# Performance work log

Hardware: AMD Instinct MI355X
Metric: run time of the kernel (lower is better)

## Reference

```python
import jax, jax.numpy as jnp
import numpy as np

C0, C1, C2 = 2000, 10000, 50000  # class cutoffs
D = 1024                          # input_size (hidden dim)
OUT_HEAD = C0 + 2                 # head output: shortlist + 2 cluster logits


def setup_inputs() -> dict:
    key = jax.random.key(0)
    ks = jax.random.split(key, 7)
    s = lambda fan_in: 1.0 / np.sqrt(fan_in)
    x = jax.random.normal(ks[0], (4096, D), dtype=jnp.float32)
    Wh = jax.random.normal(ks[1], (OUT_HEAD, D), dtype=jnp.float32) * s(D)
    bh = jnp.zeros((OUT_HEAD,), dtype=jnp.float32)
    # tail 0: D -> D//4**0 -> (C1-C0)
    W0a = jax.random.normal(ks[2], (D, D), dtype=jnp.float32) * s(D)
    W0b = jax.random.normal(ks[3], (C1 - C0, D), dtype=jnp.float32) * s(D)
    # tail 1: D -> D//4**1 -> (C2-C1)
    W1a = jax.random.normal(ks[4], (D // 4, D), dtype=jnp.float32) * s(D)
    W1b = jax.random.normal(ks[5], (C2 - C1, D // 4), dtype=jnp.float32) * s(D // 4)
    return {"x": x, "Wh": Wh, "bh": bh, "W0a": W0a, "W0b": W0b, "W1a": W1a, "W1b": W1b}


def reference(x, Wh, bh, W0a, W0b, W1a, W1b):
    # head: [B, OUT_HEAD]; log-softmax over shortlist + cluster logits
    lsm_head = jax.nn.log_softmax(x @ Wh.T + bh, axis=-1)
    # tail clusters: capacity-reduction linear, projection, log-softmax within cluster
    lsm_t0 = jax.nn.log_softmax((x @ W0a.T) @ W0b.T, axis=-1)  # [B, C1-C0]
    lsm_t1 = jax.nn.log_softmax((x @ W1a.T) @ W1b.T, axis=-1)  # [B, C2-C1]
    # flat log-probs: cluster log-prob broadcast-added to within-cluster log-probs
    prob = jnp.concatenate([
        lsm_head[:, :C0],
        lsm_head[:, C0:C0 + 1] + lsm_t0,
        lsm_head[:, C0 + 1:C0 + 2] + lsm_t1,
    ], axis=1)  # [B, C2]
    return prob
```

## Files before the change

### kernel.cpp

```cpp
#include <hip/hip_runtime.h>
#include <hip/hip_bf16.h>
#include <math.h>

#define CC0 2000
#define CC1 10000
#define CC2 50000
#define DH  1024
#define BATCH 4096
#define OUT_HEAD (CC0 + 2)

#define N0_P 8192
#define N1_P 40192
#define NH_P 2048

typedef __attribute__((ext_vector_type(4))) float  f32x4;
typedef __attribute__((ext_vector_type(8))) __bf16 bf16x8;
typedef __attribute__((ext_vector_type(8))) short  s16x8;

__device__ __forceinline__ void gload_lds16(const void* g, void* l) {
    __builtin_amdgcn_global_load_lds(
        (const __attribute__((address_space(1))) void*)g,
        (__attribute__((address_space(3))) void*)l, 16, 0, 0);
}

__global__ __launch_bounds__(256) void convert_all_kernel(
    const float4* __restrict__ s0, ushort4* __restrict__ d0, int n0s, int n0d,
    const float4* __restrict__ s1, ushort4* __restrict__ d1, int n1s, int n1d,
    const float4* __restrict__ s2, ushort4* __restrict__ d2, int n2s, int n2d,
    const float4* __restrict__ s3, ushort4* __restrict__ d3, int n3s, int n3d,
    const float4* __restrict__ s4, ushort4* __restrict__ d4, int n4s, int n4d,
    const float4* __restrict__ s5, ushort4* __restrict__ d5, int n5s, int n5d,
    float* __restrict__ rs0, float* __restrict__ rs1)
{
    if (blockIdx.y == 6) {
        int i = blockIdx.x * blockDim.x + threadIdx.x;
        if (i < BATCH) { rs0[i] = 0.f; rs1[i] = 0.f; }
        return;
    }
    const float4* src; ushort4* dst; int ns, nd;
    switch (blockIdx.y) {
        case 0: src = s0; dst = d0; ns = n0s; nd = n0d; break;
        case 1: src = s1; dst = d1; ns = n1s; nd = n1d; break;
        case 2: src = s2; dst = d2; ns = n2s; nd = n2d; break;
        case 3: src = s3; dst = d3; ns = n3s; nd = n3d; break;
        case 4: src = s4; dst = d4; ns = n4s; nd = n4d; break;
        default: src = s5; dst = d5; ns = n5s; nd = n5d; break;
    }
    int i = blockIdx.x * blockDim.x + threadIdx.x;
    const int stride = gridDim.x * blockDim.x;
    for (; i < nd; i += stride) {
        ushort4 o = {0, 0, 0, 0};
        if (i < ns) {
            float4 v = src[i];
            o.x = __builtin_bit_cast(unsigned short, (__bf16)v.x);
            o.y = __builtin_bit_cast(unsigned short, (__bf16)v.y);
            o.z = __builtin_bit_cast(unsigned short, (__bf16)v.z);
            o.w = __builtin_bit_cast(unsigned short, (__bf16)v.w);
        }
        dst[i] = o;
    }
}

__global__ __launch_bounds__(256) void gemm128x3_kernel(
    const ushort* __restrict__ x_bf,
    const ushort* __restrict__ W0a_bf, ushort* __restrict__ h0,
    const ushort* __restrict__ W1a_bf, ushort* __restrict__ h1,
    const ushort* __restrict__ Wh_bf,  float*  __restrict__ headL)
{
    __shared__ ushort As[128 * 64];
    __shared__ ushort Bs[128 * 64];

    const int gb = blockIdx.x;
    const ushort* B; void* C;
    int N, ldC, wmode, nbx, lin;
    const int K = DH;
    if (gb < 256)      { B = W0a_bf; C = h0;    N = DH;       ldC = DH;       wmode = 1; nbx = 8;  lin = gb; }
    else if (gb < 320) { B = W1a_bf; C = h1;    N = 256;      ldC = 256;      wmode = 1; nbx = 2;  lin = gb - 256; }
    else               { B = Wh_bf;  C = headL; N = OUT_HEAD; ldC = OUT_HEAD; wmode = 2; nbx = 16; lin = gb - 320; }

    const int nwg = nbx * 32;
    const int q = nwg >> 3;
    int bid = (lin & 7) * q + (lin >> 3);
    const int bx = bid % nbx;
    const int by = bid / nbx;

    const int t = threadIdx.x;
    const int lane = t & 63;
    const int w = t >> 6;
    const int wr = w >> 1, wc = w & 1;
    const int lr = lane & 15;
    const int lg = lane >> 4;
    const int bm = by * 128;
    const int bn = bx * 128;
    const int lrow = lane >> 3;
    const int lcol = (lane & 7) * 8;

    f32x4 acc[4][4] = {};

    for (int k0 = 0; k0 < K; k0 += 64) {
        #pragma unroll
        for (int i = 0; i < 4; ++i) {
            const int seg = w * 4 + i;
            const int row = seg * 8 + lrow;
            gload_lds16(x_bf + (size_t)(bm + row) * K + k0 + lcol, &As[seg * 512]);
            gload_lds16(B + (size_t)(bn + row) * K + k0 + lcol, &Bs[seg * 512]);
        }
        __syncthreads();
        #pragma unroll
        for (int ks = 0; ks < 2; ++ks) {
            s16x8 af[4], bfr[4];
            #pragma unroll
            for (int m = 0; m < 4; ++m)
                af[m] = *(const s16x8*)&As[(wr * 64 + m * 16 + lr) * 64 + ks * 32 + lg * 8];
            #pragma unroll
            for (int n = 0; n < 4; ++n)
                bfr[n] = *(const s16x8*)&Bs[(wc * 64 + n * 16 + lr) * 64 + ks * 32 + lg * 8];
            #pragma unroll
            for (int m = 0; m < 4; ++m)
                #pragma unroll
                for (int n = 0; n < 4; ++n)
                    acc[m][n] = __builtin_amdgcn_mfma_f32_16x16x32_bf16(
                        __builtin_bit_cast(bf16x8, af[m]),
                        __builtin_bit_cast(bf16x8, bfr[n]), acc[m][n], 0, 0, 0);
        }
        __syncthreads();
    }

    #pragma unroll
    for (int m = 0; m < 4; ++m)
        #pragma unroll
        for (int r = 0; r < 4; ++r) {
            const int row = bm + wr * 64 + m * 16 + lg * 4 + r;
            #pragma unroll
            for (int n = 0; n < 4; ++n) {
                const int col = bn + wc * 64 + n * 16 + lr;
                float v = acc[m][n][r];
                if (col < N) {
                    if (wmode == 1)
                        ((ushort*)C)[(size_t)row * ldC + col] =
                            __builtin_bit_cast(unsigned short, (__bf16)v);
                    else
                        ((float*)C)[(size_t)row * ldC + col] = v;
                }
            }
        }
}

__global__ __launch_bounds__(512, 1) void tails256_kernel(
    const ushort* __restrict__ h0, const ushort* __restrict__ W0b,
    ushort* __restrict__ L0, float* __restrict__ rs0,
    const ushort* __restrict__ h1, const ushort* __restrict__ W1b,
    ushort* __restrict__ L1, float* __restrict__ rs1)
{
    __shared__ ushort lds[2][2][256 * 64];

    const int gb = blockIdx.x;
    const ushort *A, *B; ushort* C; float* rsum;
    int K, N, nbx, ldC, lin;
    if (gb < 512) { A = h0; B = W0b; C = L0; rsum = rs0; K = DH;  N = CC1 - CC0; nbx = N0_P / 256; ldC = N0_P; lin = gb; }
    else          { A = h1; B = W1b; C = L1; rsum = rs1; K = 256; N = CC2 - CC1; nbx = N1_P / 256; ldC = N1_P; lin = gb - 512; }

    const int nwg = nbx * 16;
    const int q8 = nwg >> 3;
    int bid = (lin & 7) * q8 + (lin >> 3);
    const int by = bid % 16;
    const int bx = bid / 16;
    const int bm = by * 256, bn = bx * 256;

    const int t = threadIdx.x;
    const int lane = t & 63;
    const int w = t >> 6;
    const int wr = w >> 2;
    const int wc = w & 3;
    const int lr = lane & 15;
    const int lg = lane >> 4;
    const int xr = (lr & 7) << 4;
    const int c0 = w * 64 + lane;

    f32x4 acc[8][4] = {};
    const int nkt = K / 64;

    auto stage_chunk = [&](int ktile, int buf, int p) {
        const int k0 = ktile * 64;
        const int mat = (p == 1 || p == 2) ? 1 : 0;
        const int j = p >> 1;
        const ushort* gbase = mat ? B : A;
        const int brow = mat ? bn : bm;
        #pragma unroll
        for (int i = 0; i < 2; ++i) {
            const int v = i * 512 + c0;
            const int vrow = v >> 3;
            int ar;
            if (mat == 0) ar = ((vrow >> 6) << 7) + (j << 6) + (vrow & 63);
            else          ar = ((vrow >> 5) << 6) + (j << 5) + (vrow & 31);
            const int cc = (v & 7) ^ (ar & 7);
            const int v0 = (i * 512 + w * 64) >> 3;
            int ar0;
            if (mat == 0) ar0 = ((v0 >> 6) << 7) + (j << 6) + (v0 & 63);
            else          ar0 = ((v0 >> 5) << 6) + (j << 5) + (v0 & 31);
            gload_lds16(gbase + (size_t)(brow + ar) * K + k0 + cc * 8,
                        (char*)&lds[buf][mat][0] + ar0 * 128);
        }
    };

    #pragma unroll
    for (int p = 0; p < 4; ++p) stage_chunk(0, 0, p);
    asm volatile("s_waitcnt vmcnt(0)" ::: "memory");
    __builtin_amdgcn_s_barrier();
    asm volatile("" ::: "memory");

    for (int tk = 0; tk < nkt; ++tk) {
        const int cur = tk & 1;
        const char* baseA = (const char*)&lds[cur][0][0];
        const char* baseB = (const char*)&lds[cur][1][0];
        const bool more = (tk + 1 < nkt);
        #pragma unroll
        for (int p = 0; p < 4; ++p) {
            const int mh = p >> 1, nh = p & 1;
            if (more) {
                stage_chunk(tk + 1, cur ^ 1, p);
                asm volatile("s_waitcnt vmcnt(6)" ::: "memory");
            } else {
                if (p == 0)      asm volatile("s_waitcnt vmcnt(4)" ::: "memory");
                else if (p == 1) asm volatile("s_waitcnt vmcnt(2)" ::: "memory");
                else if (p == 2) asm volatile("s_waitcnt vmcnt(0)" ::: "memory");
            }
            __builtin_amdgcn_s_barrier();
            asm volatile("" ::: "memory");

            s16x8 af[4][2], bq[2][2];
            #pragma unroll
            for (int m_ = 0; m_ < 4; ++m_) {
                const int row = wr * 128 + (mh * 4 + m_) * 16 + lr;
                #pragma unroll
                for (int ks = 0; ks < 2; ++ks)
                    af[m_][ks] = *(const s16x8*)(baseA + (row * 128 + ((ks * 64 + lg * 16) ^ xr)));
            }
            #pragma unroll
            for (int n_ = 0; n_ < 2; ++n_) {
                const int row = wc * 64 + (nh * 2 + n_) * 16 + lr;
                #pragma unroll
                for (int ks = 0; ks < 2; ++ks)
                    bq[n_][ks] = *(const s16x8*)(baseB + (row * 128 + ((ks * 64 + lg * 16) ^ xr)));
            }
            __builtin_amdgcn_s_setprio(1);
            #pragma unroll
            for (int m_ = 0; m_ < 4; ++m_)
                #pragma unroll
                for (int n_ = 0; n_ < 2; ++n_)
                    #pragma unroll
                    for (int ks = 0; ks < 2; ++ks)
                        acc[mh * 4 + m_][nh * 2 + n_] = __builtin_amdgcn_mfma_f32_16x16x32_bf16(
                            __builtin_bit_cast(bf16x8, af[m_][ks]),
                            __builtin_bit_cast(bf16x8, bq[n_][ks]),
                            acc[mh * 4 + m_][nh * 2 + n_], 0, 0, 0);
            __builtin_amdgcn_s_setprio(0);
        }
    }

    #pragma unroll
    for (int m = 0; m < 8; ++m) {
        #pragma unroll
        for (int r = 0; r < 4; ++r) {
            const int row = bm + wr * 128 + m * 16 + lg * 4 + r;
            float psum = 0.f;
            #pragma unroll
            for (int n = 0; n < 4; ++n) {
                const int col = bn + wc * 64 + n * 16 + lr;
                float v = acc[m][n][r];
                if (col < N) {
                    C[(size_t)row * ldC + col] =
                        __builtin_bit_cast(unsigned short, (__bf16)v);
                    psum += __expf(v);
                }
            }
            #pragma unroll
            for (int mm = 1; mm < 16; mm <<= 1) psum += __shfl_xor(psum, mm, 64);
            if (lr == 0) atomicAdd(&rsum[row], psum);
        }
    }
}

__global__ __launch_bounds__(256) void head_lsm_kernel(
    const float* __restrict__ HL, const float* __restrict__ bh,
    float* __restrict__ out, float* __restrict__ s01)
{
    const int row = blockIdx.x;
    const float* L = HL + (size_t)row * OUT_HEAD;
    const int t = threadIdx.x;
    __shared__ float red[4];

    float m = -1e30f;
    for (int i = t; i < OUT_HEAD; i += 256) m = fmaxf(m, L[i] + bh[i]);
    #pragma unroll
    for (int s = 1; s < 64; s <<= 1) m = fmaxf(m, __shfl_xor(m, s, 64));
    if ((t & 63) == 0) red[t >> 6] = m;
    __syncthreads();
    m = fmaxf(fmaxf(red[0], red[1]), fmaxf(red[2], red[3]));

    float sum = 0.f;
    for (int i = t; i < OUT_HEAD; i += 256) sum += __expf(L[i] + bh[i] - m);
    #pragma unroll
    for (int s = 1; s < 64; s <<= 1) sum += __shfl_xor(sum, s, 64);
    __syncthreads();
    if ((t & 63) == 0) red[t >> 6] = sum;
    __syncthreads();
    const float lse = m + logf(red[0] + red[1] + red[2] + red[3]);

    float* orow = out + (size_t)row * CC2;
    for (int i = t; i < CC0; i += 256) orow[i] = L[i] + bh[i] - lse;
    if (t == 0) {
        s01[2 * row + 0] = L[CC0 + 0] + bh[CC0 + 0] - lse;
        s01[2 * row + 1] = L[CC0 + 1] + bh[CC0 + 1] - lse;
    }
}

__global__ __launch_bounds__(256) void prep_add_kernel(
    const float* __restrict__ s01, const float* __restrict__ rs0,
    const float* __restrict__ rs1, float* __restrict__ add0,
    float* __restrict__ add1, int n)
{
    int i = blockIdx.x * blockDim.x + threadIdx.x;
    if (i < n) {
        add0[i] = s01[2 * i + 0] - logf(rs0[i]);
        add1[i] = s01[2 * i + 1] - logf(rs1[i]);
    }
}

__global__ __launch_bounds__(256) void finalize_all_kernel(
    const ushort* __restrict__ L0, const ushort* __restrict__ L1,
    const float* __restrict__ add0, const float* __restrict__ add1,
    float* __restrict__ out)
{
    const int row = blockIdx.y;
    const int c = blockIdx.x * blockDim.x + threadIdx.x;
    const ushort* src; float* dst; float add;
    if (c < 1000) {
        src = L0 + (size_t)row * N0_P + c * 8;
        dst = out + (size_t)row * CC2 + CC0 + c * 8;
        add = add0[row];
    } else if (c < 6000) {
        const int c1 = c - 1000;
        src = L1 + (size_t)row * N1_P + c1 * 8;
        dst = out + (size_t)row * CC2 + CC1 + c1 * 8;
        add = add1[row];
    } else return;
    s16x8 v = *(const s16x8*)src;
    float4 o0, o1;
    o0.x = __builtin_bit_cast(float, (unsigned)(unsigned short)v[0] << 16) + add;
    o0.y = __builtin_bit_cast(float, (unsigned)(unsigned short)v[1] << 16) + add;
    o0.z = __builtin_bit_cast(float, (unsigned)(unsigned short)v[2] << 16) + add;
    o0.w = __builtin_bit_cast(float, (unsigned)(unsigned short)v[3] << 16) + add;
    o1.x = __builtin_bit_cast(float, (unsigned)(unsigned short)v[4] << 16) + add;
    o1.y = __builtin_bit_cast(float, (unsigned)(unsigned short)v[5] << 16) + add;
    o1.z = __builtin_bit_cast(float, (unsigned)(unsigned short)v[6] << 16) + add;
    o1.w = __builtin_bit_cast(float, (unsigned)(unsigned short)v[7] << 16) + add;
    *(float4*)dst = o0;
    *(float4*)(dst + 4) = o1;
}

extern "C" void kernel_launch(void* const* d_in, const int* in_sizes, int n_in,
                              void* d_out, int out_size, void* d_ws, size_t ws_size,
                              hipStream_t stream) {
    const float* x   = (const float*)d_in[0];
    const float* Wh  = (const float*)d_in[1];
    const float* bh  = (const float*)d_in[2];
    const float* W0a = (const float*)d_in[3];
    const float* W0b = (const float*)d_in[4];
    const float* W1a = (const float*)d_in[5];
    const float* W1b = (const float*)d_in[6];
    float* out = (float*)d_out;
    char*  ws  = (char*)d_ws;

    size_t off = 0;
    auto alloc = [&](size_t bytes) { size_t o = off; off += (bytes + 255) & ~(size_t)255; return o; };
    ushort* x_bf   = (ushort*)(ws + alloc((size_t)BATCH * DH * 2));
    ushort* Wh_bf  = (ushort*)(ws + alloc((size_t)NH_P * DH * 2));
    ushort* W0a_bf = (ushort*)(ws + alloc((size_t)DH * DH * 2));
    ushort* W0b_bf = (ushort*)(ws + alloc((size_t)N0_P * DH * 2));
    ushort* W1a_bf = (ushort*)(ws + alloc((size_t)256 * DH * 2));
    ushort* W1b_bf = (ushort*)(ws + alloc((size_t)N1_P * 256 * 2));
    ushort* h0_bf  = (ushort*)(ws + alloc((size_t)BATCH * DH * 2));
    ushort* h1_bf  = (ushort*)(ws + alloc((size_t)BATCH * 256 * 2));
    float*  headL  = (float*)(ws + alloc((size_t)BATCH * OUT_HEAD * 4));
    float*  s01    = (float*)(ws + alloc((size_t)BATCH * 2 * 4));
    float*  rs0    = (float*)(ws + alloc((size_t)BATCH * 4));
    float*  rs1    = (float*)(ws + alloc((size_t)BATCH * 4));
    float*  add0   = (float*)(ws + alloc((size_t)BATCH * 4));
    float*  add1   = (float*)(ws + alloc((size_t)BATCH * 4));
    ushort* L0     = (ushort*)(ws + alloc((size_t)BATCH * N0_P * 2));
    ushort* L1     = (ushort*)(ws + alloc((size_t)BATCH * N1_P * 2));

    convert_all_kernel<<<dim3(1280, 7), 256, 0, stream>>>(
        (const float4*)x,   (ushort4*)x_bf,   BATCH * DH / 4,        BATCH * DH / 4,
        (const float4*)Wh,  (ushort4*)Wh_bf,  OUT_HEAD * DH / 4,     NH_P * DH / 4,
        (const float4*)W0a, (ushort4*)W0a_bf, DH * DH / 4,           DH * DH / 4,
        (const float4*)W0b, (ushort4*)W0b_bf, (CC1 - CC0) * DH / 4,  N0_P * DH / 4,
        (const float4*)W1a, (ushort4*)W1a_bf, 256 * DH / 4,          256 * DH / 4,
        (const float4*)W1b, (ushort4*)W1b_bf, (CC2 - CC1) * 256 / 4, N1_P * 256 / 4,
        rs0, rs1);

    gemm128x3_kernel<<<832, 256, 0, stream>>>(
        x_bf, W0a_bf, h0_bf, W1a_bf, h1_bf, Wh_bf, headL);

    head_lsm_kernel<<<BATCH, 256, 0, stream>>>(headL, bh, out, s01);

    tails256_kernel<<<512 + (N1_P / 256) * 16, 512, 0, stream>>>(
        h0_bf, W0b_bf, L0, rs0, h1_bf, W1b_bf, L1, rs1);

    prep_add_kernel<<<(BATCH + 255) / 256, 256, 0, stream>>>(s01, rs0, rs1, add0, add1, BATCH);

    finalize_all_kernel<<<dim3(24, BATCH), 256, 0, stream>>>(L0, L1, add0, add1, out);
}
```

Before: 606.1 us.

## Move tail exp-sum out of GEMM epilogue into a per-row finalize kernel

The tail GEMM no longer computes exp and atomically accumulates row sums in its epilogue. A new per-row finalize kernel reads the bf16 logits, reduces the exp-sum, computes the log-normaliser and writes the output, replacing the prep_add and finalize kernels and the zero-init blocks. The GEMM inner loop also keeps B fragments across the four sub-steps, so A and B are not re-read from LDS. This removes atomics and epilogue transcendental work, but each row's logits are now read twice in the finalize pass and sums are taken over bf16-rounded values.

Result: no change. 600.4 us (-0.9%).

```diff
diff --git a/kernel.cpp b/kernel.cpp
--- a/kernel.cpp
+++ b/kernel.cpp
@@ -29,14 +29,8 @@
     const float4* __restrict__ s2, ushort4* __restrict__ d2, int n2s, int n2d,
     const float4* __restrict__ s3, ushort4* __restrict__ d3, int n3s, int n3d,
     const float4* __restrict__ s4, ushort4* __restrict__ d4, int n4s, int n4d,
-    const float4* __restrict__ s5, ushort4* __restrict__ d5, int n5s, int n5d,
-    float* __restrict__ rs0, float* __restrict__ rs1)
+    const float4* __restrict__ s5, ushort4* __restrict__ d5, int n5s, int n5d)
 {
-    if (blockIdx.y == 6) {
-        int i = blockIdx.x * blockDim.x + threadIdx.x;
-        if (i < BATCH) { rs0[i] = 0.f; rs1[i] = 0.f; }
-        return;
-    }
     const float4* src; ushort4* dst; int ns, nd;
     switch (blockIdx.y) {
         case 0: src = s0; dst = d0; ns = n0s; nd = n0d; break;
@@ -148,17 +142,17 @@
 
 __global__ __launch_bounds__(512, 1) void tails256_kernel(
     const ushort* __restrict__ h0, const ushort* __restrict__ W0b,
-    ushort* __restrict__ L0, float* __restrict__ rs0,
+    ushort* __restrict__ L0,
     const ushort* __restrict__ h1, const ushort* __restrict__ W1b,
-    ushort* __restrict__ L1, float* __restrict__ rs1)
+    ushort* __restrict__ L1)
 {
     __shared__ ushort lds[2][2][256 * 64];
 
     const int gb = blockIdx.x;
-    const ushort *A, *B; ushort* C; float* rsum;
+    const ushort *A, *B; ushort* C;
     int K, N, nbx, ldC, lin;
-    if (gb < 512) { A = h0; B = W0b; C = L0; rsum = rs0; K = DH;  N = CC1 - CC0; nbx = N0_P / 256; ldC = N0_P; lin = gb; }
-    else          { A = h1; B = W1b; C = L1; rsum = rs1; K = 256; N = CC2 - CC1; nbx = N1_P / 256; ldC = N1_P; lin = gb - 512; }
+    if (gb < 512) { A = h0; B = W0b; C = L0; K = DH;  N = CC1 - CC0; nbx = N0_P / 256; ldC = N0_P; lin = gb; }
+    else          { A = h1; B = W1b; C = L1; K = 256; N = CC2 - CC1; nbx = N1_P / 256; ldC = N1_P; lin = gb - 512; }
 
     const int nwg = nbx * 16;
     const int q8 = nwg >> 3;
@@ -183,7 +177,7 @@
     auto stage_chunk = [&](int ktile, int buf, int p) {
         const int k0 = ktile * 64;
         const int mat = (p == 1 || p == 2) ? 1 : 0;
-        const int j = p >> 1;
+        const int j = (p == 3) ? 1 : (p == 2 ? 1 : 0);
         const ushort* gbase = mat ? B : A;
         const int brow = mat ? bn : bm;
         #pragma unroll
@@ -214,6 +208,10 @@
         const char* baseA = (const char*)&lds[cur][0][0];
         const char* baseB = (const char*)&lds[cur][1][0];
         const bool more = (tk + 1 < nkt);
+
+        s16x8 bq[4][2];
+        s16x8 af[4][2];
+
         #pragma unroll
         for (int p = 0; p < 4; ++p) {
             const int mh = p >> 1, nh = p & 1;
@@ -228,20 +226,23 @@
             __builtin_amdgcn_s_barrier();
             asm volatile("" ::: "memory");
 
-            s16x8 af[4][2], bq[2][2];
-            #pragma unroll
-            for (int m_ = 0; m_ < 4; ++m_) {
-                const int row = wr * 128 + (mh * 4 + m_) * 16 + lr;
+            if (p == 0 || p == 2) {
                 #pragma unroll
-                for (int ks = 0; ks < 2; ++ks)
-                    af[m_][ks] = *(const s16x8*)(baseA + (row * 128 + ((ks * 64 + lg * 16) ^ xr)));
+                for (int m_ = 0; m_ < 4; ++m_) {
+                    const int row = wr * 128 + (mh * 4 + m_) * 16 + lr;
+                    #pragma unroll
+                    for (int ks = 0; ks < 2; ++ks)
+                        af[m_][ks] = *(const s16x8*)(baseA + (row * 128 + ((ks * 64 + lg * 16) ^ xr)));
+                }
             }
-            #pragma unroll
-            for (int n_ = 0; n_ < 2; ++n_) {
-                const int row = wc * 64 + (nh * 2 + n_) * 16 + lr;
+            if (p == 0 || p == 1) {
                 #pragma unroll
-                for (int ks = 0; ks < 2; ++ks)
-                    bq[n_][ks] = *(const s16x8*)(baseB + (row * 128 + ((ks * 64 + lg * 16) ^ xr)));
+                for (int n_ = 0; n_ < 2; ++n_) {
+                    const int row = wc * 64 + (p * 2 + n_) * 16 + lr;
+                    #pragma unroll
+                    for (int ks = 0; ks < 2; ++ks)
+                        bq[p * 2 + n_][ks] = *(const s16x8*)(baseB + (row * 128 + ((ks * 64 + lg * 16) ^ xr)));
+                }
             }
             __builtin_amdgcn_s_setprio(1);
             #pragma unroll
@@ -252,7 +253,7 @@
                     for (int ks = 0; ks < 2; ++ks)
                         acc[mh * 4 + m_][nh * 2 + n_] = __builtin_amdgcn_mfma_f32_16x16x32_bf16(
                             __builtin_bit_cast(bf16x8, af[m_][ks]),
-                            __builtin_bit_cast(bf16x8, bq[n_][ks]),
+                            __builtin_bit_cast(bf16x8, bq[nh * 2 + n_][ks]),
                             acc[mh * 4 + m_][nh * 2 + n_], 0, 0, 0);
             __builtin_amdgcn_s_setprio(0);
         }
@@ -263,20 +264,13 @@
         #pragma unroll
         for (int r = 0; r < 4; ++r) {
             const int row = bm + wr * 128 + m * 16 + lg * 4 + r;
-            float psum = 0.f;
             #pragma unroll
             for (int n = 0; n < 4; ++n) {
                 const int col = bn + wc * 64 + n * 16 + lr;
-                float v = acc[m][n][r];
-                if (col < N) {
+                if (col < N)
                     C[(size_t)row * ldC + col] =
-                        __builtin_bit_cast(unsigned short, (__bf16)v);
-                    psum += __expf(v);
-                }
+                        __builtin_bit_cast(unsigned short, (__bf16)acc[m][n][r]);
             }
-            #pragma unroll
-            for (int mm = 1; mm < 16; mm <<= 1) psum += __shfl_xor(psum, mm, 64);
-            if (lr == 0) atomicAdd(&rsum[row], psum);
         }
     }
 }
@@ -315,48 +309,65 @@
     }
 }
 
-__global__ __launch_bounds__(256) void prep_add_kernel(
-    const float* __restrict__ s01, const float* __restrict__ rs0,
-    const float* __restrict__ rs1, float* __restrict__ add0,
-    float* __restrict__ add1, int n)
+__global__ __launch_bounds__(512) void finalize_rows_kernel(
+    const ushort* __restrict__ L0, const ushort* __restrict__ L1,
+    const float* __restrict__ s01, float* __restrict__ out)
 {
-    int i = blockIdx.x * blockDim.x + threadIdx.x;
-    if (i < n) {
-        add0[i] = s01[2 * i + 0] - logf(rs0[i]);
-        add1[i] = s01[2 * i + 1] - logf(rs1[i]);
-    }
-}
-
-__global__ __launch_bounds__(256) void finalize_all_kernel(
-    const ushort* __restrict__ L0, const ushort* __restrict__ L1,
-    const float* __restrict__ add0, const float* __restrict__ add1,
-    float* __restrict__ out)
-{
-    const int row = blockIdx.y;
-    const int c = blockIdx.x * blockDim.x + threadIdx.x;
-    const ushort* src; float* dst; float add;
-    if (c < 1000) {
-        src = L0 + (size_t)row * N0_P + c * 8;
-        dst = out + (size_t)row * CC2 + CC0 + c * 8;
-        add = add0[row];
-    } else if (c < 6000) {
-        const int c1 = c - 1000;
-        src = L1 + (size_t)row * N1_P + c1 * 8;
-        dst = out + (size_t)row * CC2 + CC1 + c1 * 8;
-        add = add1[row];
-    } else return;
-    s16x8 v = *(const s16x8*)src;
-    float4 o0, o1;
-    o0.x = __builtin_bit_cast(float, (unsigned)(unsigned short)v[0] << 16) + add;
-    o0.y = __builtin_bit_cast(float, (unsigned)(unsigned short)v[1] << 16) + add;
-    o0.z = __builtin_bit_cast(float, (unsigned)(unsigned short)v[2] << 16) + add;
-    o0.w = __builtin_bit_cast(float, (unsigned)(unsigned short)v[3] << 16) + add;
-    o1.x = __builtin_bit_cast(float, (unsigned)(unsigned short)v[4] << 16) + add;
-    o1.y = __builtin_bit_cast(float, (unsigned)(unsigned short)v[5] << 16) + add;
-    o1.z = __builtin_bit_cast(float, (unsigned)(unsigned short)v[6] << 16) + add;
-    o1.w = __builtin_bit_cast(float, (unsigned)(unsigned short)v[7] << 16) + add;
-    *(float4*)dst = o0;
-    *(float4*)(dst + 4) = o1;
+    const int row = blockIdx.x;
+    const int t = threadIdx.x;
+    const ushort* r0 = L0 + (size_t)row * N0_P;
+    const ushort* r1 = L1 + (size_t)row * N1_P;
+
+    float p0 = 0.f, p1 = 0.f;
+    for (int c = t; c < 1000; c += 512) {
+        s16x8 v = *(const s16x8*)(r0 + c * 8);
+        #pragma unroll
+        for (int j = 0; j < 8; ++j)
+            p0 += __expf(__builtin_bit_cast(float, (unsigned)(unsigned short)v[j] << 16));
+    }
+    for (int c = t; c < 5000; c += 512) {
+        s16x8 v = *(const s16x8*)(r1 + c * 8);
+        #pragma unroll
+        for (int j = 0; j < 8; ++j)
+            p1 += __expf(__builtin_bit_cast(float, (unsigned)(unsigned short)v[j] << 16));
+    }
+    #pragma unroll
+    for (int s = 1; s < 64; s <<= 1) {
+        p0 += __shfl_xor(p0, s, 64);
+        p1 += __shfl_xor(p1, s, 64);
+    }
+    __shared__ float red0[8], red1[8], bc[2];
+    if ((t & 63) == 0) { red0[t >> 6] = p0; red1[t >> 6] = p1; }
+    __syncthreads();
+    if (t == 0) {
+        float s0 = 0.f, s1 = 0.f;
+        #pragma unroll
+        for (int i = 0; i < 8; ++i) { s0 += red0[i]; s1 += red1[i]; }
+        bc[0] = s01[2 * row + 0] - logf(s0);
+        bc[1] = s01[2 * row + 1] - logf(s1);
+    }
+    __syncthreads();
+    const float a0 = bc[0], a1 = bc[1];
+
+    float* o = out + (size_t)row * CC2;
+    for (int c = t; c < 6000; c += 512) {
+        const bool t0 = c < 1000;
+        const ushort* src = t0 ? r0 + c * 8 : r1 + (size_t)(c - 1000) * 8;
+        float* dst = t0 ? o + CC0 + c * 8 : o + CC1 + (c - 1000) * 8;
+        const float add = t0 ? a0 : a1;
+        s16x8 v = *(const s16x8*)src;
+        float4 o0, o1;
+        o0.x = __builtin_bit_cast(float, (unsigned)(unsigned short)v[0] << 16) + add;
+        o0.y = __builtin_bit_cast(float, (unsigned)(unsigned short)v[1] << 16) + add;
+        o0.z = __builtin_bit_cast(float, (unsigned)(unsigned short)v[2] << 16) + add;
+        o0.w = __builtin_bit_cast(float, (unsigned)(unsigned short)v[3] << 16) + add;
+        o1.x = __builtin_bit_cast(float, (unsigned)(unsigned short)v[4] << 16) + add;
+        o1.y = __builtin_bit_cast(float, (unsigned)(unsigned short)v[5] << 16) + add;
+        o1.z = __builtin_bit_cast(float, (unsigned)(unsigned short)v[6] << 16) + add;
+        o1.w = __builtin_bit_cast(float, (unsigned)(unsigned short)v[7] << 16) + add;
+        *(float4*)dst = o0;
+        *(float4*)(dst + 4) = o1;
+    }
 }
 
 extern "C" void kernel_launch(void* const* d_in, const int* in_sizes, int n_in,
@@ -384,21 +395,16 @@
     ushort* h1_bf  = (ushort*)(ws + alloc((size_t)BATCH * 256 * 2));
     float*  headL  = (float*)(ws + alloc((size_t)BATCH * OUT_HEAD * 4));
     float*  s01    = (float*)(ws + alloc((size_t)BATCH * 2 * 4));
-    float*  rs0    = (float*)(ws + alloc((size_t)BATCH * 4));
-    float*  rs1    = (float*)(ws + alloc((size_t)BATCH * 4));
-    float*  add0   = (float*)(ws + alloc((size_t)BATCH * 4));
-    float*  add1   = (float*)(ws + alloc((size_t)BATCH * 4));
     ushort* L0     = (ushort*)(ws + alloc((size_t)BATCH * N0_P * 2));
     ushort* L1     = (ushort*)(ws + alloc((size_t)BATCH * N1_P * 2));
 
-    convert_all_kernel<<<dim3(1280, 7), 256, 0, stream>>>(
+    convert_all_kernel<<<dim3(1280, 6), 256, 0, stream>>>(
         (const float4*)x,   (ushort4*)x_bf,   BATCH * DH / 4,        BATCH * DH / 4,
         (const float4*)Wh,  (ushort4*)Wh_bf,  OUT_HEAD * DH / 4,     NH_P * DH / 4,
         (const float4*)W0a, (ushort4*)W0a_bf, DH * DH / 4,           DH * DH / 4,
         (const float4*)W0b, (ushort4*)W0b_bf, (CC1 - CC0) * DH / 4,  N0_P * DH / 4,
         (const float4*)W1a, (ushort4*)W1a_bf, 256 * DH / 4,          256 * DH / 4,
-        (const float4*)W1b, (ushort4*)W1b_bf, (CC2 - CC1) * 256 / 4, N1_P * 256 / 4,
-        rs0, rs1);
+        (const float4*)W1b, (ushort4*)W1b_bf, (CC2 - CC1) * 256 / 4, N1_P * 256 / 4);
 
     gemm128x3_kernel<<<832, 256, 0, stream>>>(
         x_bf, W0a_bf, h0_bf, W1a_bf, h1_bf, Wh_bf, headL);
@@ -406,9 +412,7 @@
     head_lsm_kernel<<<BATCH, 256, 0, stream>>>(headL, bh, out, s01);
 
     tails256_kernel<<<512 + (N1_P / 256) * 16, 512, 0, stream>>>(
-        h0_bf, W0b_bf, L0, rs0, h1_bf, W1b_bf, L1, rs1);
-
-    prep_add_kernel<<<(BATCH + 255) / 256, 256, 0, stream>>>(s01, rs0, rs1, add0, add1, BATCH);
-
-    finalize_all_kernel<<<dim3(24, BATCH), 256, 0, stream>>>(L0, L1, add0, add1, out);
-}
+        h0_bf, W0b_bf, L0, h1_bf, W1b_bf, L1);
+
+    finalize_rows_kernel<<<BATCH, 512, 0, stream>>>(L0, L1, s01, out);
+}
```
